# Kernel optimization log

Measured on AMD Instinct MI355X. Metric: run time of the kernel, lower is better.

## Reference

```python
import jax, jax.numpy as jnp
import numpy as np

B, N, D, H = 2, 2048, 128, 16  # batch, seq, per-head dim, heads
ALL = D * H


def setup_inputs() -> dict:
    key = jax.random.key(0)
    ks = jax.random.split(key, 12)
    s = 0.02
    x = jax.random.normal(ks[0], (B, N, D), dtype=jnp.float32)
    mask = jax.random.randint(ks[1], (B, N), 0, 2, dtype=jnp.int32)
    Wq = jax.random.normal(ks[2], (D, ALL), dtype=jnp.float32) * s
    bq = jnp.zeros((ALL,), dtype=jnp.float32)
    Wk = jax.random.normal(ks[3], (D, ALL), dtype=jnp.float32) * s
    bk = jnp.zeros((ALL,), dtype=jnp.float32)
    Wv = jax.random.normal(ks[4], (D, ALL), dtype=jnp.float32) * s
    bv = jnp.zeros((ALL,), dtype=jnp.float32)
    Wo = jax.random.normal(ks[5], (ALL, D), dtype=jnp.float32) * s
    bo = jnp.zeros((D,), dtype=jnp.float32)
    return {"x": x, "mask": mask, "Wq": Wq, "bq": bq, "Wk": Wk, "bk": bk,
            "Wv": Wv, "bv": bv, "Wo": Wo, "bo": bo}


def reference(x, mask, Wq, bq, Wk, bk, Wv, bv, Wo, bo):
    b, n, d = x.shape
    h = ALL // d
    # project and split heads: [b, n, h, d] -> [b, h, n, d]
    q = (x @ Wq + bq).reshape(b, n, h, d).transpose(0, 2, 1, 3)
    k = (x @ Wk + bk).reshape(b, n, h, d).transpose(0, 2, 1, 3)
    v = (x @ Wv + bv).reshape(b, n, h, d).transpose(0, 2, 1, 3)
    scores = jnp.einsum('bhqd,bhkd->bhqk', q, k) / jnp.sqrt(jnp.float32(d))
    # key mask: [b,1,1,n]
    scores = jnp.where(mask[:, None, None, :] == 0, -jnp.inf, scores)
    attn = jax.nn.softmax(scores, axis=-1)  # dropout p=0.0 -> identity
    out = jnp.einsum('bhqk,bhkd->bhqd', attn, v)
    # query mask: [b,1,n,1]
    out = jnp.where(mask[:, None, :, None] == 0, 0.0, out)
    out = out.transpose(0, 2, 1, 3).reshape(b, n, h * d)
    return out @ Wo + bo
```

## Files before the change

### kernel.cpp

```cpp
#include <hip/hip_runtime.h>
#include <hip/hip_bf16.h>

#define B_   2
#define N_   2048
#define D_   128
#define H_   16
#define ALL_ 2048
#define M_   (B_*N_)
#define BH_  (B_*H_)

typedef __bf16 bf16;
typedef __bf16 bf16x8 __attribute__((ext_vector_type(8)));
typedef __bf16 bf16x4 __attribute__((ext_vector_type(4)));
typedef float  floatx4 __attribute__((ext_vector_type(4)));

#define MFMA32K(a,b,c) __builtin_amdgcn_mfma_f32_16x16x32_bf16((a),(b),(c),0,0,0)

__device__ inline void load_lds16(const bf16* g, bf16* l) {
    __builtin_amdgcn_global_load_lds((const __attribute__((address_space(1))) void*)g,
                                     (__attribute__((address_space(3))) void*)l, 16, 0, 0);
}

#define WAITCNT_VM(n) ((0xF << 8) | (0x7 << 4) | (n))


__global__ __launch_bounds__(256) void prep_weights(const float* __restrict__ x,
                                                    const float* __restrict__ Wq,
                                                    const float* __restrict__ Wk,
                                                    const float* __restrict__ Wv,
                                                    const float* __restrict__ Wo,
                                                    const int* __restrict__ mask,
                                                    bf16* __restrict__ Wqf,
                                                    bf16* __restrict__ Wkf,
                                                    bf16* __restrict__ Wvf,
                                                    bf16* __restrict__ Wof,
                                                    bf16* __restrict__ xf,
                                                    float* __restrict__ mbias) {
    __shared__ bf16 pw[16896];
    int bid = blockIdx.x, t = threadIdx.x;
    int lane = t & 63, wave = t >> 6;
    int lrow = lane & 15, quad = lane >> 4;

    if (bid < 192) {
        int m = bid / 64, rest = bid % 64;
        int cg = rest >> 1, kh = rest & 1;
        const float* W = (m == 0) ? Wq : (m == 1) ? Wk : Wv;
        bf16* Wf       = (m == 0) ? Wqf : (m == 1) ? Wkf : Wvf;
        int slot = t & 15, rowb = t >> 4;
#pragma unroll
        for (int i = 0; i < 4; i++) {
            int rl_ = rowb + i * 16;
            float4 v = *(const float4*)(W + (size_t)(kh * 64 + rl_) * 2048 + cg * 64 + slot * 4);
            bf16x4 o; o[0]=(bf16)v.x; o[1]=(bf16)v.y; o[2]=(bf16)v.z; o[3]=(bf16)v.w;
            *(bf16x4*)(&pw[rl_ * 68 + slot * 4]) = o;
        }
        __syncthreads();
        int ctl = wave;
#pragma unroll
        for (int kfl = 0; kfl < 2; kfl++) {
            bf16x8 w;
#pragma unroll
            for (int j = 0; j < 8; j++) w[j] = pw[(kfl * 32 + quad * 8 + j) * 68 + ctl * 16 + lrow];
            *(bf16x8*)(Wf + (size_t)((cg * 4 + ctl) * 4 + kh * 2 + kfl) * 512 + lane * 8) = w;
        }
    } else if (bid < 224) {
        int idx = bid - 192;
        int kb16 = idx >> 1, ch = idx & 1;
        int k0 = kb16 * 128;
        int slot = t & 15, rowb = t >> 4;
#pragma unroll
        for (int i = 0; i < 8; i++) {
            int r = rowb + i * 16;
            float4 v = *(const float4*)(Wo + (size_t)(k0 + r) * 128 + ch * 64 + slot * 4);
            bf16x4 o; o[0]=(bf16)v.x; o[1]=(bf16)v.y; o[2]=(bf16)v.z; o[3]=(bf16)v.w;
            *(bf16x4*)(&pw[r * 68 + slot * 4]) = o;
        }
        __syncthreads();
        int ctl = wave;
        int ct = ch * 4 + ctl;
#pragma unroll
        for (int kfl = 0; kfl < 4; kfl++) {
            bf16x8 w;
#pragma unroll
            for (int j = 0; j < 8; j++)
                w[j] = pw[(kfl * 32 + ((j >> 2) << 4) + quad * 4 + (j & 3)) * 68 + ctl * 16 + lrow];
            *(bf16x8*)(Wof + (size_t)(ct * 64 + kb16 * 4 + kfl) * 512 + lane * 8) = w;
        }
    } else if (bid < 352) {
        int idx = bid - 224, r0 = idx * 32;
        int slot = t & 31, rowb = t >> 5;
#pragma unroll
        for (int i = 0; i < 4; i++) {
            int r = rowb + i * 8;
            float4 v = *(const float4*)(x + (size_t)(r0 + r) * 128 + slot * 4);
            bf16x4 o; o[0]=(bf16)v.x; o[1]=(bf16)v.y; o[2]=(bf16)v.z; o[3]=(bf16)v.w;
            *(bf16x4*)(&pw[r * 136 + slot * 4]) = o;
        }
        __syncthreads();
        int rtl = wave >> 1;
        int kf2 = (wave & 1) * 2;
#pragma unroll
        for (int kfl = 0; kfl < 2; kfl++) {
            int kf = kf2 + kfl;
            bf16x8 w = *(const bf16x8*)(&pw[(rtl * 16 + lrow) * 136 + kf * 32 + quad * 8]);
            *(bf16x8*)(xf + (size_t)((idx * 2 + rtl) * 4 + kf) * 512 + lane * 8) = w;
        }
    } else {
        int e = (bid - 352) * 256 + t;
        mbias[e] = mask[e] ? 0.0f : -43.2808512f;
    }
}

__global__ __launch_bounds__(256) void qkv_proj(const bf16* __restrict__ xf,
                                                const float* __restrict__ bq,
                                                const float* __restrict__ bk,
                                                const float* __restrict__ bv,
                                                const bf16* __restrict__ Wqf,
                                                const bf16* __restrict__ Wkf,
                                                const bf16* __restrict__ Wvf,
                                                bf16* __restrict__ Qf,
                                                bf16* __restrict__ Kf,
                                                bf16* __restrict__ Vf) {
    __shared__ bf16 tile[64][72];

    int tid = threadIdx.x;
    int wave = tid >> 6, lane = tid & 63;
    int lrow = lane & 15, quad = lane >> 4;
    int r0b = blockIdx.x * 64;
    int c0 = blockIdx.y * 64;
    int cg4 = c0 >> 4;

    int rt = (r0b >> 4) + wave;
    bf16x8 a[4];
#pragma unroll
    for (int kf = 0; kf < 4; kf++)
        a[kf] = *(const bf16x8*)(xf + (size_t)(rt * 4 + kf) * 512 + lane * 8);

    int bb = r0b >> 11;
    int h  = c0 >> 7;
    int bhw = bb * 16 + h;
    int tile16 = (r0b & 2047) >> 4;
    int kbt = (r0b & 2047) >> 6;
    floatx4 zero4 = {0.f, 0.f, 0.f, 0.f};

#pragma unroll
    for (int z = 0; z < 3; z++) {
        const float* bias = (z == 0) ? bq : (z == 1) ? bk : bv;
        const bf16*  Wf   = (z == 0) ? Wqf : (z == 1) ? Wkf : Wvf;

        floatx4 acc[4] = {zero4, zero4, zero4, zero4};
#pragma unroll
        for (int kf = 0; kf < 4; kf++) {
#pragma unroll
            for (int nf = 0; nf < 4; nf++) {
                bf16x8 b = *(const bf16x8*)(Wf + (size_t)((cg4 + nf) * 4 + kf) * 512 + lane * 8);
                acc[nf] = MFMA32K(a[kf], b, acc[nf]);
            }
        }

#pragma unroll
        for (int nf = 0; nf < 4; nf++) {
            int col = nf * 16 + lrow;
            float bvv = bias[c0 + col];
#pragma unroll
            for (int r = 0; r < 4; r++) {
                int row = wave * 16 + quad * 4 + r;
                bf16 val = (bf16)(acc[nf][r] + bvv);
                if (z < 2) tile[row][col] = val;
                else       tile[col][row] = val;
            }
        }
        __syncthreads();

        if (z < 2) {
            bf16* dst = (z == 0) ? Qf : Kf;
            int s = wave;
            int kfbase = (c0 & 127) >> 5;
            size_t fbase = ((size_t)bhw * 128 + tile16 + s) * 4 + kfbase;
#pragma unroll
            for (int kfl = 0; kfl < 2; kfl++) {
                bf16x8 w = *(const bf16x8*)(&tile[s * 16 + lrow][kfl * 32 + quad * 8]);
                *(bf16x8*)(dst + (fbase + kfl) * 512 + lane * 8) = w;
            }
        } else {
            int nfl = wave;
            int nfbase = (c0 & 127) >> 4;
            size_t fbase = (((size_t)bhw * 32 + kbt) * 8 + (nfbase + nfl)) * 2;
#pragma unroll
            for (int g = 0; g < 2; g++) {
                bf16x4 a0 = *(const bf16x4*)(&tile[nfl * 16 + lrow][g * 32 + quad * 4]);
                bf16x4 a1 = *(const bf16x4*)(&tile[nfl * 16 + lrow][g * 32 + 16 + quad * 4]);
                bf16x8 w;
                w[0]=a0[0]; w[1]=a0[1]; w[2]=a0[2]; w[3]=a0[3];
                w[4]=a1[0]; w[5]=a1[1]; w[6]=a1[2]; w[7]=a1[3];
                *(bf16x8*)(Vf + (fbase + g) * 512 + lane * 8) = w;
            }
        }
        if (z < 2) __syncthreads();
    }
}

__global__ __launch_bounds__(256, 2) void flash_attn(const bf16* __restrict__ Qf,
                                                     const bf16* __restrict__ Kf,
                                                     const bf16* __restrict__ Vf,
                                                     const float* __restrict__ mbias,
                                                     const int* __restrict__ mask,
                                                     bf16* __restrict__ ctxf) {
    __shared__ bf16 sm[32768];
    __shared__ float mbL[2048];

    int tid = threadIdx.x;
    int wave = tid >> 6, lane = tid & 63;
    int lrow = lane & 15, quad = lane >> 4;
    int bid = blockIdx.x;
    int xcd = bid & 7, seq = bid >> 3;
    int bh  = xcd * 4 + (seq >> 4);
    int qblk = seq & 15;
    int b  = bh >> 4;
    int q0 = qblk * 128 + wave * 32;

    const float* mbp = mbias + b * N_;
    const bf16* kbase = Kf + (size_t)bh * 262144;
    const bf16* vbase = Vf + (size_t)bh * 262144 + lane * 8;

    bf16x8 qf[2][4];
#pragma unroll
    for (int u = 0; u < 2; u++)
#pragma unroll
        for (int kf = 0; kf < 4; kf++)
            qf[u][kf] = *(const bf16x8*)(Qf + (size_t)(((size_t)bh * 128 + (q0 >> 4) + u) * 4 + kf) * 512 + lane * 8);

    bf16x8 ones;
#pragma unroll
    for (int j = 0; j < 8; j++) ones[j] = (bf16)1.0f;

    floatx4 zero4 = {0.f, 0.f, 0.f, 0.f};
    floatx4 O[2][8];
#pragma unroll
    for (int u = 0; u < 2; u++)
#pragma unroll
        for (int nf = 0; nf < 8; nf++) O[u][nf] = zero4;
    floatx4 Oext[2] = {zero4, zero4};

    const float scale = 0.12751742f;

#pragma unroll
    for (int tt = 0; tt < 3; tt++) {
#pragma unroll
        for (int i = 0; i < 4; i++) {
            int seg = wave * 4 + i;
            load_lds16(kbase + (size_t)tt * 8192 + seg * 512 + lane * 8,
                       &sm[tt * 8192 + seg * 512]);
        }
    }
#pragma unroll
    for (int i = 0; i < 2; i++) {
        int seg = wave * 2 + i;
        load_lds16((const bf16*)(mbp + seg * 256) + lane * 8, (bf16*)(mbL + seg * 256));
    }
    __builtin_amdgcn_s_waitcnt(WAITCNT_VM(0));
    __builtin_amdgcn_s_barrier();

    bf16x8 pa[2], pb[2];
#pragma unroll
    for (int s = 0; s < 4; s++) {
        floatx4 S0 = zero4, S1 = zero4;
        __builtin_amdgcn_s_setprio(1);
#pragma unroll
        for (int kf = 0; kf < 4; kf++) {
            bf16x8 kfr = *(const bf16x8*)(&sm[((s * 4 + kf) * 64 + lane) * 8]);
            S0 = MFMA32K(kfr, qf[0][kf], S0);
            S1 = MFMA32K(kfr, qf[1][kf], S1);
        }
        __builtin_amdgcn_s_setprio(0);
        float4 mb4 = *(const float4*)(mbL + s * 16 + quad * 4);
        const float* mbr = (const float*)&mb4;
        int o = (s & 1) * 4;
#pragma unroll
        for (int r = 0; r < 4; r++) {
            float p0 = __builtin_amdgcn_exp2f(fmaf(S0[r], scale, mbr[r]));
            float p1 = __builtin_amdgcn_exp2f(fmaf(S1[r], scale, mbr[r]));
            if (s < 2) { pa[0][o + r] = (bf16)p0; pa[1][o + r] = (bf16)p1; }
            else       { pb[0][o + r] = (bf16)p0; pb[1][o + r] = (bf16)p1; }
        }
    }

    for (int t = 0; t < 32; t++) {
        const bf16* vsrc = vbase + (size_t)t * 8192;
        bf16x8 vreg[16];
#pragma unroll
        for (int f = 0; f < 16; f++)
            vreg[f] = *(const bf16x8*)(vsrc + f * 512);

        if (t < 29) {
            int dst = ((t + 3) & 3) << 13;
            const bf16* ksrc = kbase + (size_t)(t + 3) * 8192;
#pragma unroll
            for (int i = 0; i < 4; i++) {
                int seg = wave * 4 + i;
                load_lds16(ksrc + seg * 512 + lane * 8, &sm[dst + seg * 512]);
            }
        }

        int nb = ((t + 1) & 3) << 13;
        int tn = t + 1;
        bf16x8 pan[2], pbn[2];
        floatx4 Sa0, Sa1, Sb0, Sb1;

        if (t < 31) {
            Sa0 = zero4; Sa1 = zero4; Sb0 = zero4; Sb1 = zero4;
            __builtin_amdgcn_s_setprio(1);
#pragma unroll
            for (int kf = 0; kf < 4; kf++) {
                bf16x8 kfr = *(const bf16x8*)(&sm[nb + ((0 * 4 + kf) * 64 + lane) * 8]);
                Sa0 = MFMA32K(kfr, qf[0][kf], Sa0);
                Sa1 = MFMA32K(kfr, qf[1][kf], Sa1);
            }
#pragma unroll
            for (int kf = 0; kf < 4; kf++) {
                bf16x8 kfr = *(const bf16x8*)(&sm[nb + ((1 * 4 + kf) * 64 + lane) * 8]);
                Sb0 = MFMA32K(kfr, qf[0][kf], Sb0);
                Sb1 = MFMA32K(kfr, qf[1][kf], Sb1);
            }
            __builtin_amdgcn_s_setprio(0);
            float4 mb4 = *(const float4*)(mbL + tn * 64 + 0 * 16 + quad * 4);
            const float* mbr = (const float*)&mb4;
#pragma unroll
            for (int r = 0; r < 4; r++) {
                pan[0][r] = (bf16)__builtin_amdgcn_exp2f(fmaf(Sa0[r], scale, mbr[r]));
                pan[1][r] = (bf16)__builtin_amdgcn_exp2f(fmaf(Sa1[r], scale, mbr[r]));
            }
        }

        __builtin_amdgcn_s_setprio(1);
        Oext[0] = MFMA32K(ones, pa[0], Oext[0]);
        Oext[1] = MFMA32K(ones, pa[1], Oext[1]);
#pragma unroll
        for (int nf = 0; nf < 8; nf++) {
            O[0][nf] = MFMA32K(vreg[nf * 2], pa[0], O[0][nf]);
            O[1][nf] = MFMA32K(vreg[nf * 2], pa[1], O[1][nf]);
        }
        __builtin_amdgcn_s_setprio(0);

        if (t < 31) {
            float4 mb4 = *(const float4*)(mbL + tn * 64 + 1 * 16 + quad * 4);
            const float* mbr = (const float*)&mb4;
#pragma unroll
            for (int r = 0; r < 4; r++) {
                pan[0][4 + r] = (bf16)__builtin_amdgcn_exp2f(fmaf(Sb0[r], scale, mbr[r]));
                pan[1][4 + r] = (bf16)__builtin_amdgcn_exp2f(fmaf(Sb1[r], scale, mbr[r]));
            }
            Sa0 = zero4; Sa1 = zero4; Sb0 = zero4; Sb1 = zero4;
            __builtin_amdgcn_s_setprio(1);
#pragma unroll
            for (int kf = 0; kf < 4; kf++) {
                bf16x8 kfr = *(const bf16x8*)(&sm[nb + ((2 * 4 + kf) * 64 + lane) * 8]);
                Sa0 = MFMA32K(kfr, qf[0][kf], Sa0);
                Sa1 = MFMA32K(kfr, qf[1][kf], Sa1);
            }
#pragma unroll
            for (int kf = 0; kf < 4; kf++) {
                bf16x8 kfr = *(const bf16x8*)(&sm[nb + ((3 * 4 + kf) * 64 + lane) * 8]);
                Sb0 = MFMA32K(kfr, qf[0][kf], Sb0);
                Sb1 = MFMA32K(kfr, qf[1][kf], Sb1);
            }
            __builtin_amdgcn_s_setprio(0);
            float4 mb4b = *(const float4*)(mbL + tn * 64 + 2 * 16 + quad * 4);
            const float* mbr2 = (const float*)&mb4b;
#pragma unroll
            for (int r = 0; r < 4; r++) {
                pbn[0][r] = (bf16)__builtin_amdgcn_exp2f(fmaf(Sa0[r], scale, mbr2[r]));
                pbn[1][r] = (bf16)__builtin_amdgcn_exp2f(fmaf(Sa1[r], scale, mbr2[r]));
            }
        }

        __builtin_amdgcn_s_setprio(1);
        Oext[0] = MFMA32K(ones, pb[0], Oext[0]);
        Oext[1] = MFMA32K(ones, pb[1], Oext[1]);
#pragma unroll
        for (int nf = 0; nf < 8; nf++) {
            O[0][nf] = MFMA32K(vreg[nf * 2 + 1], pb[0], O[0][nf]);
            O[1][nf] = MFMA32K(vreg[nf * 2 + 1], pb[1], O[1][nf]);
        }
        __builtin_amdgcn_s_setprio(0);

        if (t < 31) {
            float4 mb4 = *(const float4*)(mbL + tn * 64 + 3 * 16 + quad * 4);
            const float* mbr = (const float*)&mb4;
#pragma unroll
            for (int r = 0; r < 4; r++) {
                pbn[0][4 + r] = (bf16)__builtin_amdgcn_exp2f(fmaf(Sb0[r], scale, mbr[r]));
                pbn[1][4 + r] = (bf16)__builtin_amdgcn_exp2f(fmaf(Sb1[r], scale, mbr[r]));
            }
#pragma unroll
            for (int u = 0; u < 2; u++) { pa[u] = pan[u]; pb[u] = pbn[u]; }
        }

        __builtin_amdgcn_s_waitcnt(WAITCNT_VM(4));
        __builtin_amdgcn_s_barrier();
    }

    const int* mp = mask + b * N_;
    int h4 = (bh & 15) * 4;
    size_t qtb = (size_t)b * 128 + (q0 >> 4);
#pragma unroll
    for (int u = 0; u < 2; u++) {
        float lsum = Oext[u][0];
        int q = q0 + u * 16 + lrow;
        float rl = (mp[q] && lsum > 0.f) ? (1.0f / lsum) : 0.f;
#pragma unroll
        for (int g = 0; g < 4; g++) {
            bf16x8 w;
#pragma unroll
            for (int j = 0; j < 4; j++) {
                w[j]     = (bf16)(O[u][2 * g][j]     * rl);
                w[j + 4] = (bf16)(O[u][2 * g + 1][j] * rl);
            }
            *(bf16x8*)(ctxf + ((qtb + u) * 64 + h4 + g) * 512 + lane * 8) = w;
        }
    }
}

__global__ __launch_bounds__(128) void out_proj(const bf16* __restrict__ ctxf,
                                                const bf16* __restrict__ Wof,
                                                const float* __restrict__ bo,
                                                float* __restrict__ out) {
    __shared__ float red[512];
    int tid = threadIdx.x;
    int wave = tid >> 6, lane = tid & 63;
    int lrow = lane & 15, quad = lane >> 4;
    int bid = blockIdx.x;
    int xcd = bid & 7, idx = bid >> 3;
    int qt = xcd * 32 + (idx >> 2);
    int ct = (idx & 3) * 2;
    int r0 = qt * 16, c0 = ct * 16;

    floatx4 zero4 = {0.f, 0.f, 0.f, 0.f};
    floatx4 acc[2] = {zero4, zero4};
    const bf16* ap = ctxf + ((size_t)qt * 64 + wave * 32) * 512 + lane * 8;
    const bf16* b0 = Wof + ((size_t)ct * 64 + wave * 32) * 512 + lane * 8;
    const bf16* b1 = b0 + (size_t)64 * 512;
#pragma unroll 4
    for (int kf = 0; kf < 32; kf++) {
        bf16x8 a  = *(const bf16x8*)(ap + (size_t)kf * 512);
        bf16x8 w0 = *(const bf16x8*)(b0 + (size_t)kf * 512);
        bf16x8 w1 = *(const bf16x8*)(b1 + (size_t)kf * 512);
        acc[0] = MFMA32K(a, w0, acc[0]);
        acc[1] = MFMA32K(a, w1, acc[1]);
    }
    if (wave == 1) {
#pragma unroll
        for (int nf = 0; nf < 2; nf++)
#pragma unroll
            for (int r = 0; r < 4; r++)
                red[nf * 256 + r * 64 + lane] = acc[nf][r];
    }
    __syncthreads();
    if (wave == 0) {
#pragma unroll
        for (int nf = 0; nf < 2; nf++) {
            int col = c0 + nf * 16 + lrow;
            float bv = bo[col];
#pragma unroll
            for (int r = 0; r < 4; r++) {
                int m = r0 + quad * 4 + r;
                out[(size_t)m * 128 + col] = acc[nf][r] + red[nf * 256 + r * 64 + lane] + bv;
            }
        }
    }
}

extern "C" void kernel_launch(void* const* d_in, const int* in_sizes, int n_in,
                              void* d_out, int out_size, void* d_ws, size_t ws_size,
                              hipStream_t stream) {
    const float* x    = (const float*)d_in[0];
    const int*   mask = (const int*)d_in[1];
    const float* Wq   = (const float*)d_in[2];
    const float* bq   = (const float*)d_in[3];
    const float* Wk   = (const float*)d_in[4];
    const float* bk   = (const float*)d_in[5];
    const float* Wv   = (const float*)d_in[6];
    const float* bv   = (const float*)d_in[7];
    const float* Wo   = (const float*)d_in[8];
    const float* bo   = (const float*)d_in[9];
    float* out = (float*)d_out;

    char* ws = (char*)d_ws;
    size_t off = 0;
    bf16* Wqf = (bf16*)(ws + off); off += (size_t)262144 * 2;
    bf16* Wkf = (bf16*)(ws + off); off += (size_t)262144 * 2;
    bf16* Wvf = (bf16*)(ws + off); off += (size_t)262144 * 2;
    bf16* Wof = (bf16*)(ws + off); off += (size_t)262144 * 2;
    bf16* xf  = (bf16*)(ws + off); off += (size_t)524288 * 2;
    size_t qkv_elems = (size_t)BH_ * N_ * 128;
    bf16* Qf  = (bf16*)(ws + off); off += qkv_elems * 2;
    bf16* Kf  = (bf16*)(ws + off); off += qkv_elems * 2;
    bf16* Vf  = (bf16*)(ws + off); off += qkv_elems * 2;
    bf16* ctxf = (bf16*)(ws + off); off += (size_t)M_ * ALL_ * 2;
    float* mbias = (float*)(ws + off); off += (size_t)B_ * N_ * 4;
    (void)ws_size; (void)in_sizes; (void)n_in; (void)out_size;

    prep_weights<<<368, 256, 0, stream>>>(x, Wq, Wk, Wv, Wo, mask,
                                          Wqf, Wkf, Wvf, Wof, xf, mbias);

    qkv_proj<<<dim3(64, 32), 256, 0, stream>>>(xf, bq, bk, bv, Wqf, Wkf, Wvf,
                                               Qf, Kf, Vf);

    flash_attn<<<512, 256, 0, stream>>>(Qf, Kf, Vf, mbias, mask, ctxf);

    out_proj<<<1024, 128, 0, stream>>>(ctxf, Wof, bo, out);
}
```

Measured before the change: 176.4 us.

## Fuse all four kernels into one persistent kernel with grid barriers

Merges weight/input prep, QKV projection, flash attention and output projection into a single 512-block kernel separated by atomic-counter grid barriers, replacing three kernel launch boundaries. The QKV and out-projection stages are remapped so that each block handles several virtual tiles. This removes launch gaps and tail drains between stages. In exchange it adds spin-wait barrier costs and a memset launch, requires all 512 blocks to be co-resident (two per CU), and makes the later stages share a single 72KB shared-memory allocation, which may lower occupancy in the lighter stages.

Measured after the change: 545.3 us. +209.2%, slower.

```diff
diff --git a/kernel.cpp b/kernel.cpp
--- a/kernel.cpp
+++ b/kernel.cpp
@@ -23,448 +23,442 @@
 
 #define WAITCNT_VM(n) ((0xF << 8) | (0x7 << 4) | (n))
 
-
-__global__ __launch_bounds__(256) void prep_weights(const float* __restrict__ x,
-                                                    const float* __restrict__ Wq,
-                                                    const float* __restrict__ Wk,
-                                                    const float* __restrict__ Wv,
-                                                    const float* __restrict__ Wo,
-                                                    const int* __restrict__ mask,
-                                                    bf16* __restrict__ Wqf,
-                                                    bf16* __restrict__ Wkf,
-                                                    bf16* __restrict__ Wvf,
-                                                    bf16* __restrict__ Wof,
-                                                    bf16* __restrict__ xf,
-                                                    float* __restrict__ mbias) {
-    __shared__ bf16 pw[16896];
-    int bid = blockIdx.x, t = threadIdx.x;
-    int lane = t & 63, wave = t >> 6;
+__device__ inline void gbar(unsigned* cnt, unsigned target) {
+    __syncthreads();
+    __threadfence();
+    if (threadIdx.x == 0) {
+        __hip_atomic_fetch_add(cnt, 1u, __ATOMIC_RELEASE, __HIP_MEMORY_SCOPE_AGENT);
+        while (__hip_atomic_load(cnt, __ATOMIC_ACQUIRE, __HIP_MEMORY_SCOPE_AGENT) < target)
+            __builtin_amdgcn_s_sleep(2);
+    }
+    __syncthreads();
+    __threadfence();
+}
+
+__global__ __launch_bounds__(256, 2) void fused_mha(
+        const float* __restrict__ x,   const int* __restrict__ mask,
+        const float* __restrict__ Wq,  const float* __restrict__ bq,
+        const float* __restrict__ Wk,  const float* __restrict__ bk,
+        const float* __restrict__ Wv,  const float* __restrict__ bv,
+        const float* __restrict__ Wo,  const float* __restrict__ bo,
+        float* __restrict__ out,
+        bf16* __restrict__ Wqf, bf16* __restrict__ Wkf, bf16* __restrict__ Wvf,
+        bf16* __restrict__ Wof, bf16* __restrict__ xf,
+        bf16* __restrict__ Qf,  bf16* __restrict__ Kf,  bf16* __restrict__ Vf,
+        bf16* __restrict__ ctxf, float* __restrict__ mbias,
+        unsigned* __restrict__ syncc)
+{
+    __shared__ __align__(16) char smem[73728];
+
+    int bid = blockIdx.x, tid = threadIdx.x;
+    int lane = tid & 63, wave = tid >> 6;
     int lrow = lane & 15, quad = lane >> 4;
-
-    if (bid < 192) {
-        int m = bid / 64, rest = bid % 64;
-        int cg = rest >> 1, kh = rest & 1;
-        const float* W = (m == 0) ? Wq : (m == 1) ? Wk : Wv;
-        bf16* Wf       = (m == 0) ? Wqf : (m == 1) ? Wkf : Wvf;
-        int slot = t & 15, rowb = t >> 4;
-#pragma unroll
-        for (int i = 0; i < 4; i++) {
-            int rl_ = rowb + i * 16;
-            float4 v = *(const float4*)(W + (size_t)(kh * 64 + rl_) * 2048 + cg * 64 + slot * 4);
-            bf16x4 o; o[0]=(bf16)v.x; o[1]=(bf16)v.y; o[2]=(bf16)v.z; o[3]=(bf16)v.w;
-            *(bf16x4*)(&pw[rl_ * 68 + slot * 4]) = o;
-        }
-        __syncthreads();
-        int ctl = wave;
-#pragma unroll
-        for (int kfl = 0; kfl < 2; kfl++) {
-            bf16x8 w;
-#pragma unroll
-            for (int j = 0; j < 8; j++) w[j] = pw[(kfl * 32 + quad * 8 + j) * 68 + ctl * 16 + lrow];
-            *(bf16x8*)(Wf + (size_t)((cg * 4 + ctl) * 4 + kh * 2 + kfl) * 512 + lane * 8) = w;
-        }
-    } else if (bid < 224) {
-        int idx = bid - 192;
-        int kb16 = idx >> 1, ch = idx & 1;
-        int k0 = kb16 * 128;
-        int slot = t & 15, rowb = t >> 4;
-#pragma unroll
-        for (int i = 0; i < 8; i++) {
-            int r = rowb + i * 16;
-            float4 v = *(const float4*)(Wo + (size_t)(k0 + r) * 128 + ch * 64 + slot * 4);
-            bf16x4 o; o[0]=(bf16)v.x; o[1]=(bf16)v.y; o[2]=(bf16)v.z; o[3]=(bf16)v.w;
-            *(bf16x4*)(&pw[r * 68 + slot * 4]) = o;
-        }
-        __syncthreads();
-        int ctl = wave;
-        int ct = ch * 4 + ctl;
-#pragma unroll
-        for (int kfl = 0; kfl < 4; kfl++) {
-            bf16x8 w;
-#pragma unroll
-            for (int j = 0; j < 8; j++)
-                w[j] = pw[(kfl * 32 + ((j >> 2) << 4) + quad * 4 + (j & 3)) * 68 + ctl * 16 + lrow];
-            *(bf16x8*)(Wof + (size_t)(ct * 64 + kb16 * 4 + kfl) * 512 + lane * 8) = w;
-        }
-    } else if (bid < 352) {
-        int idx = bid - 224, r0 = idx * 32;
-        int slot = t & 31, rowb = t >> 5;
-#pragma unroll
-        for (int i = 0; i < 4; i++) {
-            int r = rowb + i * 8;
-            float4 v = *(const float4*)(x + (size_t)(r0 + r) * 128 + slot * 4);
-            bf16x4 o; o[0]=(bf16)v.x; o[1]=(bf16)v.y; o[2]=(bf16)v.z; o[3]=(bf16)v.w;
-            *(bf16x4*)(&pw[r * 136 + slot * 4]) = o;
-        }
-        __syncthreads();
-        int rtl = wave >> 1;
-        int kf2 = (wave & 1) * 2;
-#pragma unroll
-        for (int kfl = 0; kfl < 2; kfl++) {
-            int kf = kf2 + kfl;
-            bf16x8 w = *(const bf16x8*)(&pw[(rtl * 16 + lrow) * 136 + kf * 32 + quad * 8]);
-            *(bf16x8*)(xf + (size_t)((idx * 2 + rtl) * 4 + kf) * 512 + lane * 8) = w;
-        }
-    } else {
-        int e = (bid - 352) * 256 + t;
-        mbias[e] = mask[e] ? 0.0f : -43.2808512f;
+    floatx4 zero4 = {0.f, 0.f, 0.f, 0.f};
+
+    {
+        bf16* pw = (bf16*)smem;
+        if (bid < 192) {
+            int m = bid / 64, rest = bid % 64;
+            int cgp = rest >> 1, kh = rest & 1;
+            const float* W = (m == 0) ? Wq : (m == 1) ? Wk : Wv;
+            bf16* Wf       = (m == 0) ? Wqf : (m == 1) ? Wkf : Wvf;
+            int slot = tid & 15, rowb = tid >> 4;
+#pragma unroll
+            for (int i = 0; i < 4; i++) {
+                int rl_ = rowb + i * 16;
+                float4 v = *(const float4*)(W + (size_t)(kh * 64 + rl_) * 2048 + cgp * 64 + slot * 4);
+                bf16x4 o; o[0]=(bf16)v.x; o[1]=(bf16)v.y; o[2]=(bf16)v.z; o[3]=(bf16)v.w;
+                *(bf16x4*)(&pw[rl_ * 68 + slot * 4]) = o;
+            }
+            __syncthreads();
+            int ctl = wave;
+#pragma unroll
+            for (int kfl = 0; kfl < 2; kfl++) {
+                bf16x8 w;
+#pragma unroll
+                for (int j = 0; j < 8; j++) w[j] = pw[(kfl * 32 + quad * 8 + j) * 68 + ctl * 16 + lrow];
+                *(bf16x8*)(Wf + (size_t)((cgp * 4 + ctl) * 4 + kh * 2 + kfl) * 512 + lane * 8) = w;
+            }
+        } else if (bid < 224) {
+            int idx = bid - 192;
+            int kb16 = idx >> 1, ch = idx & 1;
+            int k0 = kb16 * 128;
+            int slot = tid & 15, rowb = tid >> 4;
+#pragma unroll
+            for (int i = 0; i < 8; i++) {
+                int r = rowb + i * 16;
+                float4 v = *(const float4*)(Wo + (size_t)(k0 + r) * 128 + ch * 64 + slot * 4);
+                bf16x4 o; o[0]=(bf16)v.x; o[1]=(bf16)v.y; o[2]=(bf16)v.z; o[3]=(bf16)v.w;
+                *(bf16x4*)(&pw[r * 68 + slot * 4]) = o;
+            }
+            __syncthreads();
+            int ctl = wave;
+            int ct = ch * 4 + ctl;
+#pragma unroll
+            for (int kfl = 0; kfl < 4; kfl++) {
+                bf16x8 w;
+#pragma unroll
+                for (int j = 0; j < 8; j++)
+                    w[j] = pw[(kfl * 32 + ((j >> 2) << 4) + quad * 4 + (j & 3)) * 68 + ctl * 16 + lrow];
+                *(bf16x8*)(Wof + (size_t)(ct * 64 + kb16 * 4 + kfl) * 512 + lane * 8) = w;
+            }
+        } else if (bid < 352) {
+            int idx = bid - 224, r0 = idx * 32;
+            int slot = tid & 31, rowb = tid >> 5;
+#pragma unroll
+            for (int i = 0; i < 4; i++) {
+                int r = rowb + i * 8;
+                float4 v = *(const float4*)(x + (size_t)(r0 + r) * 128 + slot * 4);
+                bf16x4 o; o[0]=(bf16)v.x; o[1]=(bf16)v.y; o[2]=(bf16)v.z; o[3]=(bf16)v.w;
+                *(bf16x4*)(&pw[r * 136 + slot * 4]) = o;
+            }
+            __syncthreads();
+            int rtl = wave >> 1;
+            int kf2 = (wave & 1) * 2;
+#pragma unroll
+            for (int kfl = 0; kfl < 2; kfl++) {
+                int kf = kf2 + kfl;
+                bf16x8 w = *(const bf16x8*)(&pw[(rtl * 16 + lrow) * 136 + kf * 32 + quad * 8]);
+                *(bf16x8*)(xf + (size_t)((idx * 2 + rtl) * 4 + kf) * 512 + lane * 8) = w;
+            }
+        } else if (bid < 368) {
+            int e = (bid - 352) * 256 + tid;
+            mbias[e] = mask[e] ? 0.0f : -43.2808512f;
+        }
     }
-}
-
-__global__ __launch_bounds__(256) void qkv_proj(const bf16* __restrict__ xf,
-                                                const float* __restrict__ bq,
-                                                const float* __restrict__ bk,
-                                                const float* __restrict__ bv,
-                                                const bf16* __restrict__ Wqf,
-                                                const bf16* __restrict__ Wkf,
-                                                const bf16* __restrict__ Wvf,
-                                                bf16* __restrict__ Qf,
-                                                bf16* __restrict__ Kf,
-                                                bf16* __restrict__ Vf) {
-    __shared__ bf16 tile[64][72];
-
-    int tid = threadIdx.x;
-    int wave = tid >> 6, lane = tid & 63;
-    int lrow = lane & 15, quad = lane >> 4;
-    int r0b = blockIdx.x * 64;
-    int c0 = blockIdx.y * 64;
-    int cg4 = c0 >> 4;
-
-    int rt = (r0b >> 4) + wave;
-    bf16x8 a[4];
-#pragma unroll
-    for (int kf = 0; kf < 4; kf++)
-        a[kf] = *(const bf16x8*)(xf + (size_t)(rt * 4 + kf) * 512 + lane * 8);
-
-    int bb = r0b >> 11;
-    int h  = c0 >> 7;
-    int bhw = bb * 16 + h;
-    int tile16 = (r0b & 2047) >> 4;
-    int kbt = (r0b & 2047) >> 6;
-    floatx4 zero4 = {0.f, 0.f, 0.f, 0.f};
-
-#pragma unroll
-    for (int z = 0; z < 3; z++) {
-        const float* bias = (z == 0) ? bq : (z == 1) ? bk : bv;
-        const bf16*  Wf   = (z == 0) ? Wqf : (z == 1) ? Wkf : Wvf;
-
-        floatx4 acc[4] = {zero4, zero4, zero4, zero4};
-#pragma unroll
-        for (int kf = 0; kf < 4; kf++) {
-#pragma unroll
-            for (int nf = 0; nf < 4; nf++) {
-                bf16x8 b = *(const bf16x8*)(Wf + (size_t)((cg4 + nf) * 4 + kf) * 512 + lane * 8);
-                acc[nf] = MFMA32K(a[kf], b, acc[nf]);
-            }
-        }
-
-#pragma unroll
-        for (int nf = 0; nf < 4; nf++) {
-            int col = nf * 16 + lrow;
-            float bvv = bias[c0 + col];
-#pragma unroll
-            for (int r = 0; r < 4; r++) {
-                int row = wave * 16 + quad * 4 + r;
-                bf16 val = (bf16)(acc[nf][r] + bvv);
-                if (z < 2) tile[row][col] = val;
-                else       tile[col][row] = val;
-            }
-        }
-        __syncthreads();
-
-        if (z < 2) {
-            bf16* dst = (z == 0) ? Qf : Kf;
-            int s = wave;
-            int kfbase = (c0 & 127) >> 5;
-            size_t fbase = ((size_t)bhw * 128 + tile16 + s) * 4 + kfbase;
-#pragma unroll
-            for (int kfl = 0; kfl < 2; kfl++) {
-                bf16x8 w = *(const bf16x8*)(&tile[s * 16 + lrow][kfl * 32 + quad * 8]);
-                *(bf16x8*)(dst + (fbase + kfl) * 512 + lane * 8) = w;
-            }
-        } else {
-            int nfl = wave;
-            int nfbase = (c0 & 127) >> 4;
-            size_t fbase = (((size_t)bhw * 32 + kbt) * 8 + (nfbase + nfl)) * 2;
-#pragma unroll
-            for (int g = 0; g < 2; g++) {
-                bf16x4 a0 = *(const bf16x4*)(&tile[nfl * 16 + lrow][g * 32 + quad * 4]);
-                bf16x4 a1 = *(const bf16x4*)(&tile[nfl * 16 + lrow][g * 32 + 16 + quad * 4]);
-                bf16x8 w;
-                w[0]=a0[0]; w[1]=a0[1]; w[2]=a0[2]; w[3]=a0[3];
-                w[4]=a1[0]; w[5]=a1[1]; w[6]=a1[2]; w[7]=a1[3];
-                *(bf16x8*)(Vf + (fbase + g) * 512 + lane * 8) = w;
-            }
-        }
-        if (z < 2) __syncthreads();
+    gbar(&syncc[0], 512);
+
+    {
+        bf16 (*tile)[72] = (bf16(*)[72])smem;
+        for (int chunk = 0; chunk < 4; chunk++) {
+            int vb = bid * 4 + chunk;
+            int r0b = (vb & 63) * 64;
+            int c0  = (vb >> 6) * 64;
+            int cg4 = c0 >> 4;
+
+            int rt = (r0b >> 4) + wave;
+            bf16x8 a[4];
+#pragma unroll
+            for (int kf = 0; kf < 4; kf++)
+                a[kf] = *(const bf16x8*)(xf + (size_t)(rt * 4 + kf) * 512 + lane * 8);
+
+            int bb = r0b >> 11;
+            int h  = c0 >> 7;
+            int bhw = bb * 16 + h;
+            int tile16 = (r0b & 2047) >> 4;
+            int kbt = (r0b & 2047) >> 6;
+
+#pragma unroll
+            for (int z = 0; z < 3; z++) {
+                const float* bias = (z == 0) ? bq : (z == 1) ? bk : bv;
+                const bf16*  Wf   = (z == 0) ? Wqf : (z == 1) ? Wkf : Wvf;
+
+                floatx4 acc[4] = {zero4, zero4, zero4, zero4};
+#pragma unroll
+                for (int kf = 0; kf < 4; kf++) {
+#pragma unroll
+                    for (int nf = 0; nf < 4; nf++) {
+                        bf16x8 b = *(const bf16x8*)(Wf + (size_t)((cg4 + nf) * 4 + kf) * 512 + lane * 8);
+                        acc[nf] = MFMA32K(a[kf], b, acc[nf]);
+                    }
+                }
+
+#pragma unroll
+                for (int nf = 0; nf < 4; nf++) {
+                    int col = nf * 16 + lrow;
+                    float bvv = bias[c0 + col];
+#pragma unroll
+                    for (int r = 0; r < 4; r++) {
+                        int row = wave * 16 + quad * 4 + r;
+                        bf16 val = (bf16)(acc[nf][r] + bvv);
+                        if (z < 2) tile[row][col] = val;
+                        else       tile[col][row] = val;
+                    }
+                }
+                __syncthreads();
+
+                if (z < 2) {
+                    bf16* dst = (z == 0) ? Qf : Kf;
+                    int s = wave;
+                    int kfbase = (c0 & 127) >> 5;
+                    size_t fbase = ((size_t)bhw * 128 + tile16 + s) * 4 + kfbase;
+#pragma unroll
+                    for (int kfl = 0; kfl < 2; kfl++) {
+                        bf16x8 w = *(const bf16x8*)(&tile[s * 16 + lrow][kfl * 32 + quad * 8]);
+                        *(bf16x8*)(dst + (fbase + kfl) * 512 + lane * 8) = w;
+                    }
+                } else {
+                    int nfl = wave;
+                    int nfbase = (c0 & 127) >> 4;
+                    size_t fbase = (((size_t)bhw * 32 + kbt) * 8 + (nfbase + nfl)) * 2;
+#pragma unroll
+                    for (int g = 0; g < 2; g++) {
+                        bf16x4 a0 = *(const bf16x4*)(&tile[nfl * 16 + lrow][g * 32 + quad * 4]);
+                        bf16x4 a1 = *(const bf16x4*)(&tile[nfl * 16 + lrow][g * 32 + 16 + quad * 4]);
+                        bf16x8 w;
+                        w[0]=a0[0]; w[1]=a0[1]; w[2]=a0[2]; w[3]=a0[3];
+                        w[4]=a1[0]; w[5]=a1[1]; w[6]=a1[2]; w[7]=a1[3];
+                        *(bf16x8*)(Vf + (fbase + g) * 512 + lane * 8) = w;
+                    }
+                }
+                if (z < 2) __syncthreads();
+            }
+            __syncthreads();
+        }
     }
-}
-
-__global__ __launch_bounds__(256, 2) void flash_attn(const bf16* __restrict__ Qf,
-                                                     const bf16* __restrict__ Kf,
-                                                     const bf16* __restrict__ Vf,
-                                                     const float* __restrict__ mbias,
-                                                     const int* __restrict__ mask,
-                                                     bf16* __restrict__ ctxf) {
-    __shared__ bf16 sm[32768];
-    __shared__ float mbL[2048];
-
-    int tid = threadIdx.x;
-    int wave = tid >> 6, lane = tid & 63;
-    int lrow = lane & 15, quad = lane >> 4;
-    int bid = blockIdx.x;
-    int xcd = bid & 7, seq = bid >> 3;
-    int bh  = xcd * 4 + (seq >> 4);
-    int qblk = seq & 15;
-    int b  = bh >> 4;
-    int q0 = qblk * 128 + wave * 32;
-
-    const float* mbp = mbias + b * N_;
-    const bf16* kbase = Kf + (size_t)bh * 262144;
-    const bf16* vbase = Vf + (size_t)bh * 262144 + lane * 8;
-
-    bf16x8 qf[2][4];
-#pragma unroll
-    for (int u = 0; u < 2; u++)
-#pragma unroll
-        for (int kf = 0; kf < 4; kf++)
-            qf[u][kf] = *(const bf16x8*)(Qf + (size_t)(((size_t)bh * 128 + (q0 >> 4) + u) * 4 + kf) * 512 + lane * 8);
-
-    bf16x8 ones;
-#pragma unroll
-    for (int j = 0; j < 8; j++) ones[j] = (bf16)1.0f;
-
-    floatx4 zero4 = {0.f, 0.f, 0.f, 0.f};
-    floatx4 O[2][8];
-#pragma unroll
-    for (int u = 0; u < 2; u++)
-#pragma unroll
-        for (int nf = 0; nf < 8; nf++) O[u][nf] = zero4;
-    floatx4 Oext[2] = {zero4, zero4};
-
-    const float scale = 0.12751742f;
-
-#pragma unroll
-    for (int tt = 0; tt < 3; tt++) {
-#pragma unroll
-        for (int i = 0; i < 4; i++) {
-            int seg = wave * 4 + i;
-            load_lds16(kbase + (size_t)tt * 8192 + seg * 512 + lane * 8,
-                       &sm[tt * 8192 + seg * 512]);
-        }
-    }
-#pragma unroll
-    for (int i = 0; i < 2; i++) {
-        int seg = wave * 2 + i;
-        load_lds16((const bf16*)(mbp + seg * 256) + lane * 8, (bf16*)(mbL + seg * 256));
-    }
-    __builtin_amdgcn_s_waitcnt(WAITCNT_VM(0));
-    __builtin_amdgcn_s_barrier();
-
-    bf16x8 pa[2], pb[2];
-#pragma unroll
-    for (int s = 0; s < 4; s++) {
-        floatx4 S0 = zero4, S1 = zero4;
-        __builtin_amdgcn_s_setprio(1);
-#pragma unroll
-        for (int kf = 0; kf < 4; kf++) {
-            bf16x8 kfr = *(const bf16x8*)(&sm[((s * 4 + kf) * 64 + lane) * 8]);
-            S0 = MFMA32K(kfr, qf[0][kf], S0);
-            S1 = MFMA32K(kfr, qf[1][kf], S1);
-        }
-        __builtin_amdgcn_s_setprio(0);
-        float4 mb4 = *(const float4*)(mbL + s * 16 + quad * 4);
-        const float* mbr = (const float*)&mb4;
-        int o = (s & 1) * 4;
-#pragma unroll
-        for (int r = 0; r < 4; r++) {
-            float p0 = __builtin_amdgcn_exp2f(fmaf(S0[r], scale, mbr[r]));
-            float p1 = __builtin_amdgcn_exp2f(fmaf(S1[r], scale, mbr[r]));
-            if (s < 2) { pa[0][o + r] = (bf16)p0; pa[1][o + r] = (bf16)p1; }
-            else       { pb[0][o + r] = (bf16)p0; pb[1][o + r] = (bf16)p1; }
-        }
-    }
-
-    for (int t = 0; t < 32; t++) {
-        const bf16* vsrc = vbase + (size_t)t * 8192;
-        bf16x8 vreg[16];
-#pragma unroll
-        for (int f = 0; f < 16; f++)
-            vreg[f] = *(const bf16x8*)(vsrc + f * 512);
-
-        if (t < 29) {
-            int dst = ((t + 3) & 3) << 13;
-            const bf16* ksrc = kbase + (size_t)(t + 3) * 8192;
+    gbar(&syncc[1], 512);
+
+    {
+        bf16* sm = (bf16*)smem;
+        float* mbL = (float*)(smem + 65536);
+
+        int xcd = bid & 7, seq = bid >> 3;
+        int bh  = xcd * 4 + (seq >> 4);
+        int qblk = seq & 15;
+        int b  = bh >> 4;
+        int q0 = qblk * 128 + wave * 32;
+
+        const float* mbp = mbias + b * N_;
+        const bf16* kbase = Kf + (size_t)bh * 262144;
+        const bf16* vbase = Vf + (size_t)bh * 262144 + lane * 8;
+
+        bf16x8 qf[2][4];
+#pragma unroll
+        for (int u = 0; u < 2; u++)
+#pragma unroll
+            for (int kf = 0; kf < 4; kf++)
+                qf[u][kf] = *(const bf16x8*)(Qf + (size_t)(((size_t)bh * 128 + (q0 >> 4) + u) * 4 + kf) * 512 + lane * 8);
+
+        bf16x8 ones;
+#pragma unroll
+        for (int j = 0; j < 8; j++) ones[j] = (bf16)1.0f;
+
+        floatx4 O[2][8];
+#pragma unroll
+        for (int u = 0; u < 2; u++)
+#pragma unroll
+            for (int nf = 0; nf < 8; nf++) O[u][nf] = zero4;
+        floatx4 Oext[2] = {zero4, zero4};
+
+        const float scale = 0.12751742f;
+
+#pragma unroll
+        for (int tt = 0; tt < 3; tt++) {
 #pragma unroll
             for (int i = 0; i < 4; i++) {
                 int seg = wave * 4 + i;
-                load_lds16(ksrc + seg * 512 + lane * 8, &sm[dst + seg * 512]);
-            }
-        }
-
-        int nb = ((t + 1) & 3) << 13;
-        int tn = t + 1;
-        bf16x8 pan[2], pbn[2];
-        floatx4 Sa0, Sa1, Sb0, Sb1;
-
-        if (t < 31) {
-            Sa0 = zero4; Sa1 = zero4; Sb0 = zero4; Sb1 = zero4;
+                load_lds16(kbase + (size_t)tt * 8192 + seg * 512 + lane * 8,
+                           &sm[tt * 8192 + seg * 512]);
+            }
+        }
+#pragma unroll
+        for (int i = 0; i < 2; i++) {
+            int seg = wave * 2 + i;
+            load_lds16((const bf16*)(mbp + seg * 256) + lane * 8, (bf16*)(mbL + seg * 256));
+        }
+        __builtin_amdgcn_s_waitcnt(WAITCNT_VM(0));
+        __builtin_amdgcn_s_barrier();
+
+        bf16x8 pa[2], pb[2];
+#pragma unroll
+        for (int s = 0; s < 4; s++) {
+            floatx4 S0 = zero4, S1 = zero4;
             __builtin_amdgcn_s_setprio(1);
 #pragma unroll
             for (int kf = 0; kf < 4; kf++) {
-                bf16x8 kfr = *(const bf16x8*)(&sm[nb + ((0 * 4 + kf) * 64 + lane) * 8]);
-                Sa0 = MFMA32K(kfr, qf[0][kf], Sa0);
-                Sa1 = MFMA32K(kfr, qf[1][kf], Sa1);
-            }
-#pragma unroll
-            for (int kf = 0; kf < 4; kf++) {
-                bf16x8 kfr = *(const bf16x8*)(&sm[nb + ((1 * 4 + kf) * 64 + lane) * 8]);
-                Sb0 = MFMA32K(kfr, qf[0][kf], Sb0);
-                Sb1 = MFMA32K(kfr, qf[1][kf], Sb1);
+                bf16x8 kfr = *(const bf16x8*)(&sm[((s * 4 + kf) * 64 + lane) * 8]);
+                S0 = MFMA32K(kfr, qf[0][kf], S0);
+                S1 = MFMA32K(kfr, qf[1][kf], S1);
             }
             __builtin_amdgcn_s_setprio(0);
-            float4 mb4 = *(const float4*)(mbL + tn * 64 + 0 * 16 + quad * 4);
+            float4 mb4 = *(const float4*)(mbL + s * 16 + quad * 4);
             const float* mbr = (const float*)&mb4;
+            int o = (s & 1) * 4;
 #pragma unroll
             for (int r = 0; r < 4; r++) {
-                pan[0][r] = (bf16)__builtin_amdgcn_exp2f(fmaf(Sa0[r], scale, mbr[r]));
-                pan[1][r] = (bf16)__builtin_amdgcn_exp2f(fmaf(Sa1[r], scale, mbr[r]));
-            }
-        }
-
-        __builtin_amdgcn_s_setprio(1);
-        Oext[0] = MFMA32K(ones, pa[0], Oext[0]);
-        Oext[1] = MFMA32K(ones, pa[1], Oext[1]);
-#pragma unroll
-        for (int nf = 0; nf < 8; nf++) {
-            O[0][nf] = MFMA32K(vreg[nf * 2], pa[0], O[0][nf]);
-            O[1][nf] = MFMA32K(vreg[nf * 2], pa[1], O[1][nf]);
-        }
-        __builtin_amdgcn_s_setprio(0);
-
-        if (t < 31) {
-            float4 mb4 = *(const float4*)(mbL + tn * 64 + 1 * 16 + quad * 4);
-            const float* mbr = (const float*)&mb4;
-#pragma unroll
-            for (int r = 0; r < 4; r++) {
-                pan[0][4 + r] = (bf16)__builtin_amdgcn_exp2f(fmaf(Sb0[r], scale, mbr[r]));
-                pan[1][4 + r] = (bf16)__builtin_amdgcn_exp2f(fmaf(Sb1[r], scale, mbr[r]));
-            }
-            Sa0 = zero4; Sa1 = zero4; Sb0 = zero4; Sb1 = zero4;
+                float p0 = __builtin_amdgcn_exp2f(fmaf(S0[r], scale, mbr[r]));
+                float p1 = __builtin_amdgcn_exp2f(fmaf(S1[r], scale, mbr[r]));
+                if (s < 2) { pa[0][o + r] = (bf16)p0; pa[1][o + r] = (bf16)p1; }
+                else       { pb[0][o + r] = (bf16)p0; pb[1][o + r] = (bf16)p1; }
+            }
+        }
+
+        for (int t = 0; t < 32; t++) {
+            const bf16* vsrc = vbase + (size_t)t * 8192;
+            bf16x8 vreg[16];
+#pragma unroll
+            for (int f = 0; f < 16; f++)
+                vreg[f] = *(const bf16x8*)(vsrc + f * 512);
+
+            if (t < 29) {
+                int dst = ((t + 3) & 3) << 13;
+                const bf16* ksrc = kbase + (size_t)(t + 3) * 8192;
+#pragma unroll
+                for (int i = 0; i < 4; i++) {
+                    int seg = wave * 4 + i;
+                    load_lds16(ksrc + seg * 512 + lane * 8, &sm[dst + seg * 512]);
+                }
+            }
+
+            int nb = ((t + 1) & 3) << 13;
+            int tn = t + 1;
+            bf16x8 pan[2], pbn[2];
+            floatx4 Sa0, Sa1, Sb0, Sb1;
+
+            if (t < 31) {
+                Sa0 = zero4; Sa1 = zero4; Sb0 = zero4; Sb1 = zero4;
+                __builtin_amdgcn_s_setprio(1);
+#pragma unroll
+                for (int kf = 0; kf < 4; kf++) {
+                    bf16x8 kfr = *(const bf16x8*)(&sm[nb + ((0 * 4 + kf) * 64 + lane) * 8]);
+                    Sa0 = MFMA32K(kfr, qf[0][kf], Sa0);
+                    Sa1 = MFMA32K(kfr, qf[1][kf], Sa1);
+                }
+#pragma unroll
+                for (int kf = 0; kf < 4; kf++) {
+                    bf16x8 kfr = *(const bf16x8*)(&sm[nb + ((1 * 4 + kf) * 64 + lane) * 8]);
+                    Sb0 = MFMA32K(kfr, qf[0][kf], Sb0);
+                    Sb1 = MFMA32K(kfr, qf[1][kf], Sb1);
+                }
+                __builtin_amdgcn_s_setprio(0);
+                float4 mb4 = *(const float4*)(mbL + tn * 64 + 0 * 16 + quad * 4);
+                const float* mbr = (const float*)&mb4;
+#pragma unroll
+                for (int r = 0; r < 4; r++) {
+                    pan[0][r] = (bf16)__builtin_amdgcn_exp2f(fmaf(Sa0[r], scale, mbr[r]));
+                    pan[1][r] = (bf16)__builtin_amdgcn_exp2f(fmaf(Sa1[r], scale, mbr[r]));
+                }
+            }
+
             __builtin_amdgcn_s_setprio(1);
-#pragma unroll
-            for (int kf = 0; kf < 4; kf++) {
-                bf16x8 kfr = *(const bf16x8*)(&sm[nb + ((2 * 4 + kf) * 64 + lane) * 8]);
-                Sa0 = MFMA32K(kfr, qf[0][kf], Sa0);
-                Sa1 = MFMA32K(kfr, qf[1][kf], Sa1);
-            }
-#pragma unroll
-            for (int kf = 0; kf < 4; kf++) {
-                bf16x8 kfr = *(const bf16x8*)(&sm[nb + ((3 * 4 + kf) * 64 + lane) * 8]);
-                Sb0 = MFMA32K(kfr, qf[0][kf], Sb0);
-                Sb1 = MFMA32K(kfr, qf[1][kf], Sb1);
+            Oext[0] = MFMA32K(ones, pa[0], Oext[0]);
+            Oext[1] = MFMA32K(ones, pa[1], Oext[1]);
+#pragma unroll
+            for (int nf = 0; nf < 8; nf++) {
+                O[0][nf] = MFMA32K(vreg[nf * 2], pa[0], O[0][nf]);
+                O[1][nf] = MFMA32K(vreg[nf * 2], pa[1], O[1][nf]);
             }
             __builtin_amdgcn_s_setprio(0);
-            float4 mb4b = *(const float4*)(mbL + tn * 64 + 2 * 16 + quad * 4);
-            const float* mbr2 = (const float*)&mb4b;
-#pragma unroll
-            for (int r = 0; r < 4; r++) {
-                pbn[0][r] = (bf16)__builtin_amdgcn_exp2f(fmaf(Sa0[r], scale, mbr2[r]));
-                pbn[1][r] = (bf16)__builtin_amdgcn_exp2f(fmaf(Sa1[r], scale, mbr2[r]));
-            }
-        }
-
-        __builtin_amdgcn_s_setprio(1);
-        Oext[0] = MFMA32K(ones, pb[0], Oext[0]);
-        Oext[1] = MFMA32K(ones, pb[1], Oext[1]);
-#pragma unroll
-        for (int nf = 0; nf < 8; nf++) {
-            O[0][nf] = MFMA32K(vreg[nf * 2 + 1], pb[0], O[0][nf]);
-            O[1][nf] = MFMA32K(vreg[nf * 2 + 1], pb[1], O[1][nf]);
-        }
-        __builtin_amdgcn_s_setprio(0);
-
-        if (t < 31) {
-            float4 mb4 = *(const float4*)(mbL + tn * 64 + 3 * 16 + quad * 4);
-            const float* mbr = (const float*)&mb4;
-#pragma unroll
-            for (int r = 0; r < 4; r++) {
-                pbn[0][4 + r] = (bf16)__builtin_amdgcn_exp2f(fmaf(Sb0[r], scale, mbr[r]));
-                pbn[1][4 + r] = (bf16)__builtin_amdgcn_exp2f(fmaf(Sb1[r], scale, mbr[r]));
-            }
-#pragma unroll
-            for (int u = 0; u < 2; u++) { pa[u] = pan[u]; pb[u] = pbn[u]; }
-        }
-
-        __builtin_amdgcn_s_waitcnt(WAITCNT_VM(4));
-        __builtin_amdgcn_s_barrier();
+
+            if (t < 31) {
+                float4 mb4 = *(const float4*)(mbL + tn * 64 + 1 * 16 + quad * 4);
+                const float* mbr = (const float*)&mb4;
+#pragma unroll
+                for (int r = 0; r < 4; r++) {
+                    pan[0][4 + r] = (bf16)__builtin_amdgcn_exp2f(fmaf(Sb0[r], scale, mbr[r]));
+                    pan[1][4 + r] = (bf16)__builtin_amdgcn_exp2f(fmaf(Sb1[r], scale, mbr[r]));
+                }
+                Sa0 = zero4; Sa1 = zero4; Sb0 = zero4; Sb1 = zero4;
+                __builtin_amdgcn_s_setprio(1);
+#pragma unroll
+                for (int kf = 0; kf < 4; kf++) {
+                    bf16x8 kfr = *(const bf16x8*)(&sm[nb + ((2 * 4 + kf) * 64 + lane) * 8]);
+                    Sa0 = MFMA32K(kfr, qf[0][kf], Sa0);
+                    Sa1 = MFMA32K(kfr, qf[1][kf], Sa1);
+                }
+#pragma unroll
+                for (int kf = 0; kf < 4; kf++) {
+                    bf16x8 kfr = *(const bf16x8*)(&sm[nb + ((3 * 4 + kf) * 64 + lane) * 8]);
+                    Sb0 = MFMA32K(kfr, qf[0][kf], Sb0);
+                    Sb1 = MFMA32K(kfr, qf[1][kf], Sb1);
+                }
+                __builtin_amdgcn_s_setprio(0);
+                float4 mb4b = *(const float4*)(mbL + tn * 64 + 2 * 16 + quad * 4);
+                const float* mbr2 = (const float*)&mb4b;
+#pragma unroll
+                for (int r = 0; r < 4; r++) {
+                    pbn[0][r] = (bf16)__builtin_amdgcn_exp2f(fmaf(Sa0[r], scale, mbr2[r]));
+                    pbn[1][r] = (bf16)__builtin_amdgcn_exp2f(fmaf(Sa1[r], scale, mbr2[r]));
+                }
+            }
+
+            __builtin_amdgcn_s_setprio(1);
+            Oext[0] = MFMA32K(ones, pb[0], Oext[0]);
+            Oext[1] = MFMA32K(ones, pb[1], Oext[1]);
+#pragma unroll
+            for (int nf = 0; nf < 8; nf++) {
+                O[0][nf] = MFMA32K(vreg[nf * 2 + 1], pb[0], O[0][nf]);
+                O[1][nf] = MFMA32K(vreg[nf * 2 + 1], pb[1], O[1][nf]);
+            }
+            __builtin_amdgcn_s_setprio(0);
+
+            if (t < 31) {
+                float4 mb4 = *(const float4*)(mbL + tn * 64 + 3 * 16 + quad * 4);
+                const float* mbr = (const float*)&mb4;
+#pragma unroll
+                for (int r = 0; r < 4; r++) {
+                    pbn[0][4 + r] = (bf16)__builtin_amdgcn_exp2f(fmaf(Sb0[r], scale, mbr[r]));
+                    pbn[1][4 + r] = (bf16)__builtin_amdgcn_exp2f(fmaf(Sb1[r], scale, mbr[r]));
+                }
+#pragma unroll
+                for (int u = 0; u < 2; u++) { pa[u] = pan[u]; pb[u] = pbn[u]; }
+            }
+
+            __builtin_amdgcn_s_waitcnt(WAITCNT_VM(4));
+            __builtin_amdgcn_s_barrier();
+        }
+
+        const int* mp = mask + b * N_;
+        int h4 = (bh & 15) * 4;
+        size_t qtb = (size_t)b * 128 + (q0 >> 4);
+#pragma unroll
+        for (int u = 0; u < 2; u++) {
+            float lsum = Oext[u][0];
+            int q = q0 + u * 16 + lrow;
+            float rl = (mp[q] && lsum > 0.f) ? (1.0f / lsum) : 0.f;
+#pragma unroll
+            for (int g = 0; g < 4; g++) {
+                bf16x8 w;
+#pragma unroll
+                for (int j = 0; j < 4; j++) {
+                    w[j]     = (bf16)(O[u][2 * g][j]     * rl);
+                    w[j + 4] = (bf16)(O[u][2 * g + 1][j] * rl);
+                }
+                *(bf16x8*)(ctxf + ((qtb + u) * 64 + h4 + g) * 512 + lane * 8) = w;
+            }
+        }
     }
-
-    const int* mp = mask + b * N_;
-    int h4 = (bh & 15) * 4;
-    size_t qtb = (size_t)b * 128 + (q0 >> 4);
-#pragma unroll
-    for (int u = 0; u < 2; u++) {
-        float lsum = Oext[u][0];
-        int q = q0 + u * 16 + lrow;
-        float rl = (mp[q] && lsum > 0.f) ? (1.0f / lsum) : 0.f;
-#pragma unroll
-        for (int g = 0; g < 4; g++) {
-            bf16x8 w;
-#pragma unroll
-            for (int j = 0; j < 4; j++) {
-                w[j]     = (bf16)(O[u][2 * g][j]     * rl);
-                w[j + 4] = (bf16)(O[u][2 * g + 1][j] * rl);
-            }
-            *(bf16x8*)(ctxf + ((qtb + u) * 64 + h4 + g) * 512 + lane * 8) = w;
-        }
-    }
-}
-
-__global__ __launch_bounds__(128) void out_proj(const bf16* __restrict__ ctxf,
-                                                const bf16* __restrict__ Wof,
-                                                const float* __restrict__ bo,
-                                                float* __restrict__ out) {
-    __shared__ float red[512];
-    int tid = threadIdx.x;
-    int wave = tid >> 6, lane = tid & 63;
-    int lrow = lane & 15, quad = lane >> 4;
-    int bid = blockIdx.x;
-    int xcd = bid & 7, idx = bid >> 3;
-    int qt = xcd * 32 + (idx >> 2);
-    int ct = (idx & 3) * 2;
-    int r0 = qt * 16, c0 = ct * 16;
-
-    floatx4 zero4 = {0.f, 0.f, 0.f, 0.f};
-    floatx4 acc[2] = {zero4, zero4};
-    const bf16* ap = ctxf + ((size_t)qt * 64 + wave * 32) * 512 + lane * 8;
-    const bf16* b0 = Wof + ((size_t)ct * 64 + wave * 32) * 512 + lane * 8;
-    const bf16* b1 = b0 + (size_t)64 * 512;
+    gbar(&syncc[2], 512);
+
+    {
+        float* red = (float*)smem;
+        int sub = wave >> 1, w2 = wave & 1;
+        int vb = sub * 512 + bid;
+        int qt = vb & 255, cty = vb >> 8;
+        int ct = cty * 2;
+        int r0 = qt * 16, c0 = ct * 16;
+
+        floatx4 acc[2] = {zero4, zero4};
+        const bf16* ap = ctxf + ((size_t)qt * 64 + w2 * 32) * 512 + lane * 8;
+        const bf16* b0 = Wof + ((size_t)ct * 64 + w2 * 32) * 512 + lane * 8;
+        const bf16* b1 = b0 + (size_t)64 * 512;
 #pragma unroll 4
-    for (int kf = 0; kf < 32; kf++) {
-        bf16x8 a  = *(const bf16x8*)(ap + (size_t)kf * 512);
-        bf16x8 w0 = *(const bf16x8*)(b0 + (size_t)kf * 512);
-        bf16x8 w1 = *(const bf16x8*)(b1 + (size_t)kf * 512);
-        acc[0] = MFMA32K(a, w0, acc[0]);
-        acc[1] = MFMA32K(a, w1, acc[1]);
-    }
-    if (wave == 1) {
-#pragma unroll
-        for (int nf = 0; nf < 2; nf++)
-#pragma unroll
-            for (int r = 0; r < 4; r++)
-                red[nf * 256 + r * 64 + lane] = acc[nf][r];
-    }
-    __syncthreads();
-    if (wave == 0) {
-#pragma unroll
-        for (int nf = 0; nf < 2; nf++) {
-            int col = c0 + nf * 16 + lrow;
-            float bv = bo[col];
-#pragma unroll
-            for (int r = 0; r < 4; r++) {
-                int m = r0 + quad * 4 + r;
-                out[(size_t)m * 128 + col] = acc[nf][r] + red[nf * 256 + r * 64 + lane] + bv;
+        for (int kf = 0; kf < 32; kf++) {
+            bf16x8 a  = *(const bf16x8*)(ap + (size_t)kf * 512);
+            bf16x8 w0 = *(const bf16x8*)(b0 + (size_t)kf * 512);
+            bf16x8 w1 = *(const bf16x8*)(b1 + (size_t)kf * 512);
+            acc[0] = MFMA32K(a, w0, acc[0]);
+            acc[1] = MFMA32K(a, w1, acc[1]);
+        }
+        if (w2 == 1) {
+#pragma unroll
+            for (int nf = 0; nf < 2; nf++)
+#pragma unroll
+                for (int r = 0; r < 4; r++)
+                    red[sub * 512 + nf * 256 + r * 64 + lane] = acc[nf][r];
+        }
+        __syncthreads();
+        if (w2 == 0) {
+#pragma unroll
+            for (int nf = 0; nf < 2; nf++) {
+                int col = c0 + nf * 16 + lrow;
+                float bv = bo[col];
+#pragma unroll
+                for (int r = 0; r < 4; r++) {
+                    int m = r0 + quad * 4 + r;
+                    out[(size_t)m * 128 + col] =
+                        acc[nf][r] + red[sub * 512 + nf * 256 + r * 64 + lane] + bv;
+                }
             }
         }
     }
@@ -498,15 +492,12 @@
     bf16* Vf  = (bf16*)(ws + off); off += qkv_elems * 2;
     bf16* ctxf = (bf16*)(ws + off); off += (size_t)M_ * ALL_ * 2;
     float* mbias = (float*)(ws + off); off += (size_t)B_ * N_ * 4;
+    unsigned* syncc = (unsigned*)(ws + off); off += 256;
     (void)ws_size; (void)in_sizes; (void)n_in; (void)out_size;
 
-    prep_weights<<<368, 256, 0, stream>>>(x, Wq, Wk, Wv, Wo, mask,
-                                          Wqf, Wkf, Wvf, Wof, xf, mbias);
-
-    qkv_proj<<<dim3(64, 32), 256, 0, stream>>>(xf, bq, bk, bv, Wqf, Wkf, Wvf,
-                                               Qf, Kf, Vf);
-
-    flash_attn<<<512, 256, 0, stream>>>(Qf, Kf, Vf, mbias, mask, ctxf);
-
-    out_proj<<<1024, 128, 0, stream>>>(ctxf, Wof, bo, out);
+    hipMemsetAsync(syncc, 0, 3 * sizeof(unsigned), stream);
+
+    fused_mha<<<512, 256, 0, stream>>>(x, mask, Wq, bq, Wk, bk, Wv, bv, Wo, bo,
+                                       out, Wqf, Wkf, Wvf, Wof, xf,
+                                       Qf, Kf, Vf, ctxf, mbias, syncc);
 }
```
